# Performance work log

Measured on AMD Instinct MI355X. Metric: run time of the kernel, lower is better.

## Reference

```python
import jax, jax.numpy as jnp
import numpy as np

N = 8192   # num_neurons
P = 64     # num stored patterns


def setup_inputs() -> dict:
    key = jax.random.key(0)
    k1, k2 = jax.random.split(key)
    # Bipolar (+/-1) stored patterns, as in classical Hopfield usage
    X = jnp.where(jax.random.normal(k1, (N, P)) >= 0, 1.0, -1.0).astype(jnp.float32)
    # Initial (possibly corrupted) bipolar state
    state = jnp.where(jax.random.normal(k2, (N,)) >= 0, 1.0, -1.0).astype(jnp.float32)
    # Visit order for asynchronous updates (torch.randperm in original; any permutation is valid)
    perm = jnp.arange(N, dtype=jnp.int32)
    return {"X": X, "state": state, "perm": perm}


def reference(X, state, perm):
    n = X.shape[0]
    # W = X X^T / N with zero diagonal (Hebbian weights), as in __init__
    W = (X @ X.T) / n                                  # [N, N]
    W = W * (1.0 - jnp.eye(n, dtype=W.dtype))
    # Strictly sequential asynchronous update over the given permutation
    def step(s, i):
        act = jnp.dot(W[i], s)                         # dot(W[i], new_state)
        s = s.at[i].set(jnp.where(act >= 0, 1.0, -1.0).astype(s.dtype))
        return s, None
    final_state, _ = jax.lax.scan(step, state, perm)
    return final_state
```

## Files before the change

kernel.cpp:

```cpp
#include <hip/hip_runtime.h>
#include <stdint.h>


#define NB 128
typedef unsigned long long u64;
typedef unsigned u32;


__device__ __forceinline__ void glds16(const void* g, void* l) {
  __builtin_amdgcn_global_load_lds(
      (const __attribute__((address_space(1))) void*)g,
      (__attribute__((address_space(3))) void*)l, 16, 0, 0);
}

__global__ __launch_bounds__(256) void hop_prep(
    const float* __restrict__ X, const float* __restrict__ state,
    const int* __restrict__ perm, float* __restrict__ m0,
    float* __restrict__ Ysw, u64* __restrict__ sig, u64* __restrict__ sigT,
    float* __restrict__ sps)
{
  const int b = blockIdx.x, t = threadIdx.x;
  const int wv = t >> 6, ln = t & 63;
  __shared__ u64 sigL[64];
  __shared__ float red[4][64];

  float acc = 0.f;
  #pragma unroll
  for (int jj = 0; jj < 16; ++jj) {
    const int j = wv*16 + jj;
    const int r = perm[b*64 + j];
    const float sr = state[r];
    const float x = X[(size_t)r*64 + ln];
    Ysw[(size_t)b*4096 + j*64 + ((((ln >> 2) ^ (j & 7)) << 2) | (ln & 3))] = x * sr;
    u64 bb = __ballot(x < 0.f);
    if (sr < 0.f) bb = ~bb;
    if (ln == 0) { sig[b*64 + j] = bb; sigL[j] = bb; }
    acc = fmaf(x, sr, acc);
  }
  red[wv][ln] = acc;
  __syncthreads();

  {
    const u64 gs = sigL[ln];
    #pragma unroll
    for (int jj = 0; jj < 16; ++jj) {
      const int p = wv*16 + jj;
      u64 tb = __ballot((unsigned)((gs >> p) & 1ull));
      if (ln == 0) sigT[b*64 + p] = tb;
    }
  }

  if (t < 64) {
    atomicAdd(&m0[t], (red[0][t] + red[1][t]) + (red[2][t] + red[3][t]));
    sps[b*64 + t] = state[perm[b*64 + t]];
  }
}

#define STEP \
  "s_ff1_i32_b64 %[i], %[mm]\n\t" \
  "v_readlane_b32 %[t0], %[slo], %[i]\n\t" \
  "v_readlane_b32 %[t1], %[shi], %[i]\n\t" \
  "s_lshl_b64 %[bit], 1, %[i]\n\t" \
  "s_or_b64 %[flips], %[flips], %[bit]\n\t" \
  "s_lshl_b64 %[live], -2, %[i]\n\t" \
  "s_addk_i32 %[thr], 0x100\n\t" \
  "v_xor_b32 %[x0], %[t0], %[slo]\n\t" \
  "v_xor_b32 %[x1], %[t1], %[shi]\n\t" \
  "v_bcnt_u32_b32 %[c], %[x0], 0\n\t" \
  "v_bcnt_u32_b32 %[c], %[x1], %[c]\n\t" \
  "v_lshl_add_u32 %[T], %[c], 3, %[T]\n\t" \
  "v_cmp_gt_i32 vcc, %[thr], %[T]\n\t" \
  "s_and_b64 %[mm], vcc, %[live]\n\t"

#define PROCESS(YB, sg, st, rr, ss) {                                         \
  const float* Yc = (YB);                                                     \
  float q0=0.f,q1=0.f,q2=0.f,q3=0.f;                                          \
  const float4* mv4 = (const float4*)mlds;                                    \
  _Pragma("unroll")                                                           \
  for (int g = 0; g < 16; ++g) {                                              \
    const float4 yv = *(const float4*)&Yc[ybase + ((g ^ lswz) << 2)];         \
    const float4 mv = mv4[g];                                                 \
    q0 = fmaf(yv.x, mv.x, q0); q1 = fmaf(yv.y, mv.y, q1);                     \
    q2 = fmaf(yv.z, mv.z, q2); q3 = fmaf(yv.w, mv.w, q3);                     \
  }                                                                           \
  int T = ((int)((q0+q1)+(q2+q3)) << 1) - (((ss) < 0.f) ? 1 : 0);             \
  const u32 slo = (u32)(sg), shi = (u32)((sg) >> 32);                         \
  u64 flips; int thr = 128;                                                   \
  {                                                                           \
    u64 live, mm, bit; u32 i_, t0, t1, x0, x1, c;                             \
    asm volatile(                                                             \
      "s_mov_b64 %[flips], 0\n\t"                                             \
      "s_mov_b64 %[live], -1\n\t"                                             \
      "v_cmp_gt_i32 vcc, %[thr], %[T]\n\t"                                    \
      "s_and_b64 %[mm], vcc, %[live]\n\t"                                     \
      "s_cbranch_scc0 9f\n\t"                                                 \
      "1:\n\t"                                                                \
      STEP "s_cbranch_scc0 9f\n\t"                                            \
      STEP "s_cbranch_scc0 9f\n\t"                                            \
      STEP "s_cbranch_scc0 9f\n\t"                                            \
      STEP "s_cbranch_scc1 1b\n\t"                                            \
      "9:\n\t"                                                                \
      : [flips]"=&s"(flips), [live]"=&s"(live), [mm]"=&s"(mm),                \
        [bit]"=&s"(bit), [i]"=&s"(i_), [t0]"=&s"(t0), [t1]"=&s"(t1),          \
        [thr]"+s"(thr), [T]"+v"(T), [x0]"=&v"(x0), [x1]"=&v"(x1),             \
        [c]"=&v"(c)                                                           \
      : [slo]"v"(slo), [shi]"v"(shi)                                          \
      : "vcc", "scc");                                                        \
  }                                                                           \
  if (flips) {        \
    const int nf = (int)__popcll(flips);                                      \
    const int pc = (int)__popcll(flips & (st));                               \
    mreg += (float)(4*pc - 2*nf);                                             \
    mlds[lane] = mreg;                                                        \
  }                                                                           \
  out[rr] = ((flips >> lane) & 1ull) ? -(ss) : (ss);                          \
}

#define PREFETCH(BN, BUF, sg, st, rr, ss) {                                   \
  const float* ys = Ysw + (size_t)(BN)*4096 + lane*4;                         \
  _Pragma("unroll")                                                           \
  for (int it = 0; it < 16; ++it) glds16(ys + it*256, &(BUF)[it*256]);        \
  sg = sig[(BN)*64+lane]; st = sigT[(BN)*64+lane];                            \
  rr = perm[(BN)*64+lane]; ss = sps[(BN)*64+lane];                            \
}

__global__ __launch_bounds__(64) void hop_solve(
    const int* __restrict__ perm, const float* __restrict__ m0,
    const float* __restrict__ Ysw, const u64* __restrict__ sig,
    const u64* __restrict__ sigT, const float* __restrict__ sps,
    float* __restrict__ out)
{
  __shared__ __align__(16) float mlds[64];
  __shared__ __align__(16) float Ybuf[2][4096];
  const int lane = threadIdx.x;
  const int ybase = lane*64, lswz = lane & 7;

  float mreg = m0[lane];
  mlds[lane] = mreg;

  u64 sgA, stA, sgB, stB; int rA, rB; float sA, sB;
  PREFETCH(0, Ybuf[0], sgA, stA, rA, sA);
  asm volatile("s_waitcnt vmcnt(0)" ::: "memory");

  for (int bb = 0; bb < NB; bb += 2) {
    PREFETCH(bb+1, Ybuf[1], sgB, stB, rB, sB);
    PROCESS(Ybuf[0], sgA, stA, rA, sA);
    asm volatile("s_waitcnt vmcnt(1)" ::: "memory");
    if (bb + 2 < NB) PREFETCH(bb+2, Ybuf[0], sgA, stA, rA, sA);
    PROCESS(Ybuf[1], sgB, stB, rB, sB);
    asm volatile("s_waitcnt vmcnt(1)" ::: "memory");
  }
}

extern "C" void kernel_launch(void* const* d_in, const int* in_sizes, int n_in,
                              void* d_out, int out_size, void* d_ws, size_t ws_size,
                              hipStream_t stream) {
  const float* X     = (const float*)d_in[0];
  const float* state = (const float*)d_in[1];
  const int*   perm  = (const int*)d_in[2];
  float* outp = (float*)d_out;

  float* m0  = (float*)d_ws;
  float* Ysw = m0 + 64;
  u64*   sig = (u64*)(Ysw + 128*4096);
  u64*   sigT= sig + 8192;
  float* sps = (float*)(sigT + 8192);

  hipMemsetAsync(m0, 0, 64*sizeof(float), stream);
  hop_prep<<<dim3(NB), dim3(256), 0, stream>>>(X, state, perm, m0, Ysw, sig, sigT, sps);
  hop_solve<<<dim3(1), dim3(64), 0, stream>>>(perm, m0, Ysw, sig, sigT, sps, outp);
}
```

Baseline: 389.6 us.

## Replace serial flip scan with Jacobi-style fixed-point iteration over flip set

Replaces the hand-written sequential scalar loop, which finds each flipping neuron in turn, with a parallel fixed-point iteration. Each step guesses the full flip set by ballot, recomputes every lane's threshold from the earlier flips, and repeats until the set stops changing, capped at six iterations. If it does not converge it falls back to a sequential scan written in C. This aims to shorten the serial dependency chain inside each 64-row block. The cost is extra readlane and popcount work per iteration, and the compiler-generated code may be slower than the inline asm.

New measurement: 385.5 us. No clear change (-1.0%).

```diff
diff --git a/kernel.cpp b/kernel.cpp
--- a/kernel.cpp
+++ b/kernel.cpp
@@ -56,64 +56,86 @@
   }
 }
 
-#define STEP \
-  "s_ff1_i32_b64 %[i], %[mm]\n\t" \
-  "v_readlane_b32 %[t0], %[slo], %[i]\n\t" \
-  "v_readlane_b32 %[t1], %[shi], %[i]\n\t" \
-  "s_lshl_b64 %[bit], 1, %[i]\n\t" \
-  "s_or_b64 %[flips], %[flips], %[bit]\n\t" \
-  "s_lshl_b64 %[live], -2, %[i]\n\t" \
-  "s_addk_i32 %[thr], 0x100\n\t" \
-  "v_xor_b32 %[x0], %[t0], %[slo]\n\t" \
-  "v_xor_b32 %[x1], %[t1], %[shi]\n\t" \
-  "v_bcnt_u32_b32 %[c], %[x0], 0\n\t" \
-  "v_bcnt_u32_b32 %[c], %[x1], %[c]\n\t" \
-  "v_lshl_add_u32 %[T], %[c], 3, %[T]\n\t" \
-  "v_cmp_gt_i32 vcc, %[thr], %[T]\n\t" \
-  "s_and_b64 %[mm], vcc, %[live]\n\t"
+__device__ __forceinline__ int corr_term(u32 slo, u32 shi, int i) {
+  const u32 a = (u32)__builtin_amdgcn_readlane((int)slo, i);
+  const u32 b = (u32)__builtin_amdgcn_readlane((int)shi, i);
+  return __popc(slo ^ a) + __popc(shi ^ b);
+}
 
-#define PROCESS(YB, sg, st, rr, ss) {                                         \
-  const float* Yc = (YB);                                                     \
-  float q0=0.f,q1=0.f,q2=0.f,q3=0.f;                                          \
-  const float4* mv4 = (const float4*)mlds;                                    \
-  _Pragma("unroll")                                                           \
-  for (int g = 0; g < 16; ++g) {                                              \
-    const float4 yv = *(const float4*)&Yc[ybase + ((g ^ lswz) << 2)];         \
-    const float4 mv = mv4[g];                                                 \
-    q0 = fmaf(yv.x, mv.x, q0); q1 = fmaf(yv.y, mv.y, q1);                     \
-    q2 = fmaf(yv.z, mv.z, q2); q3 = fmaf(yv.w, mv.w, q3);                     \
-  }                                                                           \
-  int T = ((int)((q0+q1)+(q2+q3)) << 1) - (((ss) < 0.f) ? 1 : 0);             \
-  const u32 slo = (u32)(sg), shi = (u32)((sg) >> 32);                         \
-  u64 flips; int thr = 128;                                                   \
-  {                                                                           \
-    u64 live, mm, bit; u32 i_, t0, t1, x0, x1, c;                             \
-    asm volatile(                                                             \
-      "s_mov_b64 %[flips], 0\n\t"                                             \
-      "s_mov_b64 %[live], -1\n\t"                                             \
-      "v_cmp_gt_i32 vcc, %[thr], %[T]\n\t"                                    \
-      "s_and_b64 %[mm], vcc, %[live]\n\t"                                     \
-      "s_cbranch_scc0 9f\n\t"                                                 \
-      "1:\n\t"                                                                \
-      STEP "s_cbranch_scc0 9f\n\t"                                            \
-      STEP "s_cbranch_scc0 9f\n\t"                                            \
-      STEP "s_cbranch_scc0 9f\n\t"                                            \
-      STEP "s_cbranch_scc1 1b\n\t"                                            \
-      "9:\n\t"                                                                \
-      : [flips]"=&s"(flips), [live]"=&s"(live), [mm]"=&s"(mm),                \
-        [bit]"=&s"(bit), [i]"=&s"(i_), [t0]"=&s"(t0), [t1]"=&s"(t1),          \
-        [thr]"+s"(thr), [T]"+v"(T), [x0]"=&v"(x0), [x1]"=&v"(x1),             \
-        [c]"=&v"(c)                                                           \
-      : [slo]"v"(slo), [shi]"v"(shi)                                          \
-      : "vcc", "scc");                                                        \
-  }                                                                           \
-  if (flips) {        \
-    const int nf = (int)__popcll(flips);                                      \
-    const int pc = (int)__popcll(flips & (st));                               \
-    mreg += (float)(4*pc - 2*nf);                                             \
-    mlds[lane] = mreg;                                                        \
-  }                                                                           \
-  out[rr] = ((flips >> lane) & 1ull) ? -(ss) : (ss);                          \
+__device__ __forceinline__ void process_block(
+    const float* __restrict__ Yc, const u64 sg, const u64 st,
+    const int rr, const float ss, float* mlds, float& mreg,
+    float* __restrict__ out, const int lane, const int ybase, const int lswz)
+{
+  float q0=0.f,q1=0.f,q2=0.f,q3=0.f;
+  const float4* mv4 = (const float4*)mlds;
+  #pragma unroll
+  for (int g = 0; g < 16; ++g) {
+    const float4 yv = *(const float4*)&Yc[ybase + ((g ^ lswz) << 2)];
+    const float4 mv = mv4[g];
+    q0 = fmaf(yv.x, mv.x, q0); q1 = fmaf(yv.y, mv.y, q1);
+    q2 = fmaf(yv.z, mv.z, q2); q3 = fmaf(yv.w, mv.w, q3);
+  }
+  const int U0 = (((int)((q0+q1)+(q2+q3))) << 1) - ((ss < 0.f) ? 1 : 0) - 128;
+  const u32 slo = (u32)sg, shi = (u32)(sg >> 32);
+
+  u64 F = __ballot(U0 < 0);
+  u64 flips = 0ull;
+  if (F) {
+    int Ub = U0;
+    {
+      int acc0 = 0, acc1 = 0;
+      u64 rem = F;
+      while (rem) {
+        const int i = (int)__builtin_ctzll(rem); rem &= rem - 1ull;
+        const int pc = corr_term(slo, shi, i);
+        acc0 += (lane > i) ? pc : 0;
+        if (rem) {
+          const int i2 = (int)__builtin_ctzll(rem); rem &= rem - 1ull;
+          const int pc2 = corr_term(slo, shi, i2);
+          acc1 += (lane > i2) ? pc2 : 0;
+        }
+      }
+      const int cnt = (int)__builtin_amdgcn_mbcnt_hi(
+          (u32)(F >> 32), __builtin_amdgcn_mbcnt_lo((u32)F, 0u));
+      Ub += ((acc0 + acc1) << 3) - (cnt << 8);
+    }
+    bool conv = false;
+    for (int it = 0; it < 6; ++it) {
+      const u64 Fn = __ballot(Ub < 0);
+      if (Fn == F) { conv = true; break; }
+      u64 dd = Fn ^ F;
+      while (dd) {
+        const int i = (int)__builtin_ctzll(dd); dd &= dd - 1ull;
+        const int pc8 = (corr_term(slo, shi, i) << 3) - 256;
+        const int d = ((Fn >> i) & 1ull) ? pc8 : -pc8;
+        Ub += (lane > i) ? d : 0;
+      }
+      F = Fn;
+    }
+    if (conv) {
+      flips = F;
+    } else {
+      int Us = U0;
+      u64 live = ~0ull;
+      u64 mm = __ballot(Us < 0);
+      while (mm) {
+        const int i = (int)__builtin_ctzll(mm);
+        flips |= (1ull << i);
+        live = (i < 63) ? ((~0ull) << (i + 1)) : 0ull;
+        Us += (corr_term(slo, shi, i) << 3) - 256;
+        mm = __ballot(Us < 0) & live;
+      }
+    }
+  }
+
+  if (flips) {
+    const int nf = (int)__popcll(flips);
+    const int pc = (int)__popcll(flips & st);
+    mreg += (float)(4*pc - 2*nf);
+    mlds[lane] = mreg;
+  }
+  out[rr] = ((flips >> lane) & 1ull) ? -ss : ss;
 }
 
 #define PREFETCH(BN, BUF, sg, st, rr, ss) {                                   \
@@ -144,10 +166,10 @@
 
   for (int bb = 0; bb < NB; bb += 2) {
     PREFETCH(bb+1, Ybuf[1], sgB, stB, rB, sB);
-    PROCESS(Ybuf[0], sgA, stA, rA, sA);
+    process_block(Ybuf[0], sgA, stA, rA, sA, mlds, mreg, out, lane, ybase, lswz);
     asm volatile("s_waitcnt vmcnt(1)" ::: "memory");
     if (bb + 2 < NB) PREFETCH(bb+2, Ybuf[0], sgA, stA, rA, sA);
-    PROCESS(Ybuf[1], sgB, stB, rB, sB);
+    process_block(Ybuf[1], sgB, stB, rB, sB, mlds, mreg, out, lane, ybase, lswz);
     asm volatile("s_waitcnt vmcnt(1)" ::: "memory");
   }
 }
```
